# Kernel optimization log

Hardware: AMD Instinct MI355X
Metric: run time of the kernel (lower is better)

Reference implementation:

```python
import jax, jax.numpy as jnp
import numpy as np
import math

N_ENT, N_USR, N_EDGE, C = 100000, 50000, 1000000, 64
N_FACT, N_REL, N_HOPS = 4, 10, 2
KG_HEADS = 2
TEMP = 0.2


def scatter_softmax(scores, seg, num_segments):
    m = jax.ops.segment_max(scores, seg, num_segments=num_segments)
    e = jnp.exp(scores - m[seg])
    s = jax.ops.segment_sum(e, seg, num_segments=num_segments)
    return e / (s[seg] + 1e-16)


def l2norm(x, eps=1e-12):
    n = jnp.linalg.norm(x, axis=-1, keepdims=True)
    return x / jnp.maximum(n, eps)


def setup_inputs() -> dict:
    key = jax.random.key(0)
    ks = jax.random.split(key, 12)
    return {
        "user_emb": jax.random.normal(ks[0], (N_USR, C), jnp.float32) * 0.1,
        "entity_emb": jax.random.normal(ks[1], (N_ENT, C), jnp.float32) * 0.1,
        "latent_emb": jax.random.normal(ks[2], (N_FACT, C), jnp.float32) * 0.1,
        "weight": jax.random.normal(ks[3], (N_REL - 1, C), jnp.float32) * 0.1,
        "disen_weight_att": jax.random.normal(ks[4], (N_FACT, N_REL - 1), jnp.float32) * 0.1,
        "kg_W_r": jax.random.normal(ks[5], (C, C), jnp.float32) * 0.1,
        "ui_vals": jax.random.uniform(ks[6], (N_EDGE,), jnp.float32),
        "edge_index": jax.random.randint(ks[7], (2, N_EDGE), 0, N_ENT, jnp.int64 if jax.config.read('jax_enable_x64') else jnp.int32),
        "edge_type": jax.random.randint(ks[8], (N_EDGE,), 1, N_REL, jnp.int32),
        "ui_rows": jax.random.randint(ks[9], (N_EDGE,), 0, N_USR, jnp.int32),
        "ui_cols": jax.random.randint(ks[10], (N_EDGE,), 0, N_ENT, jnp.int32),
    }


def reference(user_emb, entity_emb, latent_emb, weight, disen_weight_att,
              kg_W_r, ui_vals, edge_index, edge_type, ui_rows, ui_cols):
    head, tail = edge_index[0], edge_index[1]
    d_k = C // KG_HEADS

    # ---- _cul_cor with ind == 'mi' ----
    disen_T = disen_weight_att.T  # [R-1, F]
    nT = disen_T / jnp.linalg.norm(disen_T, axis=1, keepdims=True)
    pos = jnp.sum(nT * nT, axis=1)
    ttl = jnp.sum(disen_T @ disen_weight_att, axis=1)
    cor = -jnp.sum(jnp.log(jnp.exp(pos / TEMP) / jnp.exp(ttl / TEMP)))

    # ---- Invariant_Capture (g_mask=None) ----
    rel_emb = weight[edge_type - 1]          # [E, C]
    head_emb = entity_emb[head]              # [E, C]
    q = (head_emb @ kg_W_r).reshape(-1, KG_HEADS, d_k)
    k = (rel_emb @ kg_W_r).reshape(-1, KG_HEADS, d_k)
    score_r = ((q * k).sum(-1) / math.sqrt(d_k)).mean(-1)  # [E]
    rel_scores = scatter_softmax(score_r, head, N_ENT)
    t_emb = entity_emb[tail]
    r_emb = rel_emb * rel_scores[:, None]
    # bmm of concat(h,r) with concat(t,r) == h.t + r.r
    score_trip = (head_emb * t_emb).sum(-1) + (r_emb * r_emb).sum(-1)
    kg_mask = scatter_softmax(score_trip, head, N_ENT)  # invariant_mask [E]

    # ---- conv_compute: n_hops Aggregator layers, no dropout (eval-determinism) ----
    counts = jnp.clip(jax.ops.segment_sum(jnp.ones_like(kg_mask), head,
                                          num_segments=N_ENT), 1.0)
    disen_w = jax.nn.softmax(disen_weight_att, axis=-1) @ weight  # [F, C]

    ent, usr = entity_emb, user_emb
    ent_res, usr_res = entity_emb, user_emb
    for _ in range(N_HOPS):
        # KG aggregate: scatter_mean over head of masked tail*relation messages
        neigh = ent[tail] * weight[edge_type - 1] * kg_mask[:, None]  # [E, C]
        ent_agg = jax.ops.segment_sum(neigh, head, num_segments=N_ENT) / counts[:, None]
        # user->factor attention on current user embedding
        score = jax.nn.softmax(usr @ latent_emb.T, axis=1)[:, :, None]  # [U, F, 1]
        # sparse user aggregation: interact_mat @ ent
        u_agg = jax.ops.segment_sum(ent[ui_cols] * ui_vals[:, None], ui_rows,
                                    num_segments=N_USR)
        mix = (disen_w[None, :, :] * score).sum(axis=1)  # [U, C]
        u_agg = u_agg * mix + u_agg
        ent = l2norm(ent_agg)
        usr = l2norm(u_agg)
        ent_res = ent_res + ent
        usr_res = usr_res + usr
    return ent_res, usr_res, cor
```

## Files before the change

### kernel.cpp

```cpp
#include <hip/hip_runtime.h>
#include <math.h>

#define N_ENT 100000
#define N_USR 50000
#define N_EDGE 1000000
#define TEMPC 0.2f
#define KG_BLOCKS (N_ENT / 4)
#define UI_BLOCKS (N_USR / 4)

#define TB_BLOCKS 6250
#define CNT_BLOCKS 489
#define SC_BLOCKS 196

#define BIN_BLOCKS 245
#define NCK 391
#define NCU 196
#define FINEK_BLOCKS NCK
#define FINEU_BLOCKS NCU

#define WLS 68

typedef unsigned short ushort_t;

__device__ __forceinline__ float waveReduceSum(float x) {
#pragma unroll
  for (int d = 32; d > 0; d >>= 1) x += __shfl_xor(x, d);
  return x;
}
__device__ __forceinline__ float waveReduceMax(float x) {
#pragma unroll
  for (int d = 32; d > 0; d >>= 1) x = fmaxf(x, __shfl_xor(x, d));
  return x;
}
__device__ __forceinline__ int waveReduceSumI(int x) {
#pragma unroll
  for (int d = 32; d > 0; d >>= 1) x += __shfl_xor(x, d);
  return x;
}
__device__ __forceinline__ float bf2f(unsigned int u16) {
  union { unsigned int i; float f; } v;
  v.i = u16 << 16;
  return v.f;
}
__device__ __forceinline__ ushort_t f2bf(float f) {
  union { unsigned int i; float f; } v;
  v.f = f;
  unsigned int u = v.i;
  u = (u + 0x7FFFu + ((u >> 16) & 1u)) >> 16;
  return (ushort_t)u;
}
__device__ __forceinline__ int rl(int v, int l) { return __builtin_amdgcn_readlane(v, l); }
__device__ __forceinline__ float rlf(float v, int l) {
  return __int_as_float(__builtin_amdgcn_readlane(__float_as_int(v), l));
}

__device__ __forceinline__ float colRT(float a0, float a1, float a2, float a3,
                                       float a4, float a5, float a6, float a7,
                                       int g, int part) {
#define RED3(x) x += __shfl_xor(x, 8); x += __shfl_xor(x, 16); x += __shfl_xor(x, 32);
  RED3(a0) RED3(a1) RED3(a2) RED3(a3) RED3(a4) RED3(a5) RED3(a6) RED3(a7)
#undef RED3
  float t0 = __shfl(a0, g), t1 = __shfl(a1, g), t2 = __shfl(a2, g), t3 = __shfl(a3, g);
  float t4 = __shfl(a4, g), t5 = __shfl(a5, g), t6 = __shfl(a6, g), t7 = __shfl(a7, g);
  float r = t0;
  r = (part == 1) ? t1 : r;
  r = (part == 2) ? t2 : r;
  r = (part == 3) ? t3 : r;
  r = (part == 4) ? t4 : r;
  r = (part == 5) ? t5 : r;
  r = (part == 6) ? t6 : r;
  r = (part == 7) ? t7 : r;
  return r;
}

__global__ void k_pre(const float* __restrict__ ent0, ushort_t* __restrict__ ent0bf,
                      const int* __restrict__ head, const int* __restrict__ uir,
                      int* __restrict__ ccnt_kg, int* __restrict__ ccnt_ui,
                      const float* __restrict__ weight, const float* __restrict__ kgW,
                      const float* __restrict__ disen,
                      float* __restrict__ V, float* __restrict__ wsq,
                      float* __restrict__ dw, float* __restrict__ cor_out,
                      const float* __restrict__ user_emb, const float* __restrict__ latent,
                      float4* __restrict__ sc4a) {
  int bid = blockIdx.x;
  if (bid < TB_BLOCKS) {
    int i = bid * 256 + threadIdx.x;
    if (i < N_ENT * 16) {
      float4 v = ((const float4*)ent0)[i];
      ushort4 o;
      o.x = f2bf(v.x); o.y = f2bf(v.y); o.z = f2bf(v.z); o.w = f2bf(v.w);
      ((ushort4*)ent0bf)[i] = o;
    }
  } else if (bid < TB_BLOCKS + CNT_BLOCKS) {
    __shared__ int histK[NCK], histU[NCU];
    int tid = threadIdx.x;
    for (int i = tid; i < NCK; i += 256) histK[i] = 0;
    for (int i = tid; i < NCU; i += 256) histU[i] = 0;
    __syncthreads();
    int i0 = ((bid - TB_BLOCKS) * 256 + tid) * 8;
    if (i0 < N_EDGE) {
      int4 ha = *(const int4*)(head + i0), hb = *(const int4*)(head + i0 + 4);
      int4 ua = *(const int4*)(uir + i0), ub = *(const int4*)(uir + i0 + 4);
      atomicAdd(&histK[ha.x >> 8], 1);
      atomicAdd(&histK[ha.y >> 8], 1);
      atomicAdd(&histK[ha.z >> 8], 1);
      atomicAdd(&histK[ha.w >> 8], 1);
      atomicAdd(&histK[hb.x >> 8], 1);
      atomicAdd(&histK[hb.y >> 8], 1);
      atomicAdd(&histK[hb.z >> 8], 1);
      atomicAdd(&histK[hb.w >> 8], 1);
      atomicAdd(&histU[ua.x >> 8], 1);
      atomicAdd(&histU[ua.y >> 8], 1);
      atomicAdd(&histU[ua.z >> 8], 1);
      atomicAdd(&histU[ua.w >> 8], 1);
      atomicAdd(&histU[ub.x >> 8], 1);
      atomicAdd(&histU[ub.y >> 8], 1);
      atomicAdd(&histU[ub.z >> 8], 1);
      atomicAdd(&histU[ub.w >> 8], 1);
    }
    __syncthreads();
    for (int i = tid; i < NCK; i += 256)
      if (histK[i] > 0) atomicAdd(&ccnt_kg[i], histK[i]);
    for (int i = tid; i < NCU; i += 256)
      if (histU[i] > 0) atomicAdd(&ccnt_ui[i], histU[i]);
  } else if (bid == TB_BLOCKS + CNT_BLOCKS) {
    __shared__ float T[9 * 64];
    __shared__ float sm[4 * 9];
    int tid = threadIdx.x;
    for (int e = tid; e < 9 * 64; e += 256) {
      int r = e >> 6, d = e & 63;
      float s = 0.f;
      for (int k = 0; k < 64; ++k) s += kgW[k * 64 + d] * weight[r * 64 + k];
      T[e] = s;
    }
    if (tid < 4) {
      float m = -INFINITY;
      for (int r = 0; r < 9; ++r) m = fmaxf(m, disen[tid * 9 + r]);
      float den = 0.f;
      float ex[9];
      for (int r = 0; r < 9; ++r) { ex[r] = expf(disen[tid * 9 + r] - m); den += ex[r]; }
      for (int r = 0; r < 9; ++r) sm[tid * 9 + r] = ex[r] / den;
    }
    __syncthreads();
    for (int e = tid; e < 9 * 64; e += 256) {
      int r = e >> 6, i = e & 63;
      float s = 0.f;
      for (int d = 0; d < 64; ++d) s += kgW[i * 64 + d] * T[r * 64 + d];
      V[e] = s;
    }
    if (tid < 9) {
      float s = 0.f;
      for (int c = 0; c < 64; ++c) { float w = weight[tid * 64 + c]; s += w * w; }
      wsq[tid] = s;
    }
    for (int e = tid; e < 4 * 64; e += 256) {
      int f = e >> 6, c = e & 63;
      float s = 0.f;
      for (int r = 0; r < 9; ++r) s += sm[f * 9 + r] * weight[r * 64 + c];
      dw[e] = s;
    }
    if (tid == 0) {
// ... 179 lines not shown
    __syncthreads();
    int pre9[9];
    int deg = 0;
    if (tid < ne) {
#pragma unroll
      for (int r = 0; r < 9; ++r) { pre9[r] = deg; deg += lcnt[tid * 9 + r]; }
    }
    int x = deg;
#pragma unroll
    for (int d = 1; d < 64; d <<= 1) {
      int y = __shfl_up(x, d);
      if (lane >= d) x += y;
    }
    if (lane == 63) woff[wid] = x;
    __syncthreads();
    if (tid == 0) {
      int a = 0;
      for (int w2 = 0; w2 < 4; ++w2) { int t = woff[w2]; woff[w2] = a; a += t; }
    }
    __syncthreads();
    int ebase = cs + (x - deg) + woff[wid];
    if (tid < ne) {
      head_ptr[gb + tid] = ebase;
#pragma unroll
      for (int r = 0; r < 9; ++r) lbase[tid * 9 + r] = ebase + pre9[r];
    }
    __syncthreads();
    for (int i = tid; i < 2304; i += 256) lcnt[i] = 0;
    __syncthreads();
    for (int i = cs + tid; i < ce; i += 256) {
      unsigned int w = stage_kg[i];
      int key = (int)((w >> 24) & 255u) * 9 + (int)((w >> 20) & 15u);
      int r = atomicAdd(&lcnt[key], 1);
      packed[lbase[key] + r] = (int)(w & 0xFFFFFFu);
    }
    __syncthreads();
    if (tid < ne) {
      int ent = gb + tid;
      float a[9] = {0, 0, 0, 0, 0, 0, 0, 0, 0};
      const uint4* row = (const uint4*)(ent0bf + ((size_t)ent << 6));
#pragma unroll
      for (int q = 0; q < 8; ++q) {
        uint4 bq = row[q];
        float ch0 = bf2f(bq.x & 0xFFFFu), ch1 = bf2f(bq.x >> 16);
        float ch2 = bf2f(bq.y & 0xFFFFu), ch3 = bf2f(bq.y >> 16);
        float ch4 = bf2f(bq.z & 0xFFFFu), ch5 = bf2f(bq.z >> 16);
        float ch6 = bf2f(bq.w & 0xFFFFu), ch7 = bf2f(bq.w >> 16);
#pragma unroll
        for (int r = 0; r < 9; ++r) {
          const float4* vp = (const float4*)(Vl + r * 64 + q * 8);
          float4 v0 = vp[0], v1 = vp[1];
          float t = a[r];
          t = fmaf(ch0, v0.x, t); t = fmaf(ch1, v0.y, t);
          t = fmaf(ch2, v0.z, t); t = fmaf(ch3, v0.w, t);
          t = fmaf(ch4, v1.x, t); t = fmaf(ch5, v1.y, t);
          t = fmaf(ch6, v1.z, t); t = fmaf(ch7, v1.w, t);
          a[r] = t;
        }
      }
      const float inv2s = 0.08838834764831845f;
      int cnt[9];
#pragma unroll
      for (int r = 0; r < 9; ++r) cnt[r] = lcnt[tid * 9 + r];
      float m1 = -INFINITY;
#pragma unroll
      for (int r = 0; r < 9; ++r)
        if (cnt[r] > 0) m1 = fmaxf(m1, a[r] * inv2s);
      if (m1 == -INFINITY) {
#pragma unroll
        for (int r = 0; r < 9; ++r) rel2t[ent * 9 + r] = 0.f;
      } else {
        float den1 = 1e-16f;
#pragma unroll
        for (int r = 0; r < 9; ++r)
          if (cnt[r] > 0) den1 += (float)cnt[r] * expf(a[r] * inv2s - m1);
#pragma unroll
        for (int r = 0; r < 9; ++r) {
          float rs = expf(a[r] * inv2s - m1) / den1;
          rel2t[ent * 9 + r] = rs * rs * wsql[r];
        }
      }
    }
  } else {
    int b = blockIdx.x - FINEK_BLOCKS;
    __shared__ int lbu[256];
    __shared__ int lcu[256];
    __shared__ int woff2[4];
    lcu[tid] = 0;
    int cs = cbase_ui[b], ce = cbase_ui[b + 1];
    int gb = b << 8;
    int nu = min(256, N_USR - gb);
    __syncthreads();
    for (int i = cs + tid; i < ce; i += 256) {
      int2 d = stage_ui[i];
      atomicAdd(&lcu[(d.x >> 24) & 255], 1);
    }
    __syncthreads();
    int deg = (tid < nu) ? lcu[tid] : 0;
    int x = deg;
#pragma unroll
    for (int d = 1; d < 64; d <<= 1) {
      int y = __shfl_up(x, d);
      if (lane >= d) x += y;
    }
    if (lane == 63) woff2[wid] = x;
    __syncthreads();
    if (tid == 0) {
      int a = 0;
      for (int w2 = 0; w2 < 4; ++w2) { int t = woff2[w2]; woff2[w2] = a; a += t; }
    }
    __syncthreads();
    int ubase = cs + (x - deg) + woff2[wid];
    __syncthreads();
    if (tid < nu) {
      ui_ptr[gb + tid] = ubase;
      lbu[tid] = ubase;
    }
    lcu[tid] = 0;
    __syncthreads();
    for (int i = cs + tid; i < ce; i += 256) {
      int2 d = stage_ui[i];
      int key = (d.x >> 24) & 255;
      int r = atomicAdd(&lcu[key], 1);
      cv[lbu[key] + r] = make_int2(d.x & 0xFFFFFF, d.y);
    }
  }
}

__device__ __forceinline__ float kg_agg64(int deg, int lane, int pk, float mk,
                                          const ushort_t* __restrict__ srcbf,
                                          const float* __restrict__ wl) {
  float a0 = 0.f, a1 = 0.f, a2 = 0.f, a3 = 0.f;
  int j = 0;
  for (; j + 4 <= deg; j += 4) {
    int p0 = rl(pk, j), p1 = rl(pk, j + 1), p2 = rl(pk, j + 2), p3 = rl(pk, j + 3);
    float k0 = rlf(mk, j), k1 = rlf(mk, j + 1), k2 = rlf(mk, j + 2), k3 = rlf(mk, j + 3);
    float r0 = bf2f(srcbf[((p0 & 0xFFFFF) << 6) + lane]);
    float r1 = bf2f(srcbf[((p1 & 0xFFFFF) << 6) + lane]);
    float r2 = bf2f(srcbf[((p2 & 0xFFFFF) << 6) + lane]);
    float r3 = bf2f(srcbf[((p3 & 0xFFFFF) << 6) + lane]);
    a0 = fmaf(r0 * wl[((p0 >> 20) & 15) * WLS + lane], k0, a0);
    a1 = fmaf(r1 * wl[((p1 >> 20) & 15) * WLS + lane], k1, a1);
    a2 = fmaf(r2 * wl[((p2 >> 20) & 15) * WLS + lane], k2, a2);
    a3 = fmaf(r3 * wl[((p3 >> 20) & 15) * WLS + lane], k3, a3);
  }
  for (; j < deg; ++j) {
    int pj = rl(pk, j);
    float kj = rlf(mk, j);
    a0 = fmaf(bf2f(srcbf[((pj & 0xFFFFF) << 6) + lane]) * wl[((pj >> 20) & 15) * WLS + lane], kj, a0);
  }
  return (a0 + a1) + (a2 + a3);
}

__device__ __forceinline__ void ui_body(int usr, int lane,
                                        const ushort_t* __restrict__ srcbf,
                                        const float4* __restrict__ sc4,
                                        const float* __restrict__ addb,
                                        float* __restrict__ outp, float* __restrict__ nxt,
                                        const int* __restrict__ uptr,
                                        const int2* __restrict__ cv,
                                        const float* __restrict__ dwl,
                                        const float* __restrict__ latl,
                                        float4* __restrict__ sc4out) {
  float4 s4 = sc4[usr];
  float m = fmaxf(fmaxf(s4.x, s4.y), fmaxf(s4.z, s4.w));
  float e0 = expf(s4.x - m), e1 = expf(s4.y - m), e2 = expf(s4.z - m), e3 = expf(s4.w - m);
  float den = e0 + e1 + e2 + e3;
  float mix = (e0 * dwl[lane] + e1 * dwl[64 + lane] + e2 * dwl[128 + lane] + e3 * dwl[192 + lane]) / den;
  int s = uptr[usr], e = uptr[usr + 1];
  int g = lane >> 3, part = lane & 7;
  float a0 = 0.f, a1 = 0.f, a2 = 0.f, a3 = 0.f;
  float a4 = 0.f, a5 = 0.f, a6 = 0.f, a7 = 0.f;
  for (int base = s; base < e; base += 64) {
    int c = min(64, e - base);
    int2 cvl = (lane < c) ? cv[base + lane] : make_int2(0, 0);
    int cl = cvl.x;
    float vl = __int_as_float(cvl.y);
    int nch = (c + 7) >> 3;
#pragma unroll
    for (int cc = 0; cc < 8; ++cc) {
      if (cc < nch) {
        int j = (cc << 3) + g;
        int cj = __shfl(cl, j);
        float vj = __shfl(vl, j);
        uint4 b = *((const uint4*)(srcbf + ((size_t)cj << 6)) + part);
        a0 = fmaf(bf2f(b.x & 0xFFFFu), vj, a0);
        a1 = fmaf(bf2f(b.x >> 16), vj, a1);
        a2 = fmaf(bf2f(b.y & 0xFFFFu), vj, a2);
        a3 = fmaf(bf2f(b.y >> 16), vj, a3);
        a4 = fmaf(bf2f(b.z & 0xFFFFu), vj, a4);
        a5 = fmaf(bf2f(b.z >> 16), vj, a5);
        a6 = fmaf(bf2f(b.w & 0xFFFFu), vj, a6);
        a7 = fmaf(bf2f(b.w >> 16), vj, a7);
      }
    }
  }
  float acc = colRT(a0, a1, a2, a3, a4, a5, a6, a7, g, part);
  float ua = acc * mix + acc;
  float nrm = sqrtf(waveReduceSum(ua * ua));
  float val = ua / fmaxf(nrm, 1e-12f);
  size_t o = (size_t)usr * 64 + lane;
  if (nxt) nxt[o] = val;
  outp[o] = addb[o] + val;
  if (sc4out) {
    float s0 = waveReduceSum(val * latl[lane]);
    float s1 = waveReduceSum(val * latl[64 + lane]);
    float s2 = waveReduceSum(val * latl[128 + lane]);
    float s3 = waveReduceSum(val * latl[192 + lane]);
    if (lane == 0) sc4out[usr] = make_float4(s0, s1, s2, s3);
  }
}

__global__ void k_mask_kg_ui(const float* __restrict__ ent0,
                             const ushort_t* __restrict__ ent0bf,
                             const int* __restrict__ hptr, const int* __restrict__ packed,
                             const float* __restrict__ rel2t,
                             float* __restrict__ mask_s, const float* __restrict__ weight,
                             float* __restrict__ out_ent, ushort_t* __restrict__ ent1bf,
                             const float4* __restrict__ sc4,
                             float* __restrict__ out_usr,
                             float* __restrict__ usr1, const int* __restrict__ uptr,
                             const int2* __restrict__ cv,
                             const float* __restrict__ user_emb, const float* __restrict__ dw,
                             const float* __restrict__ latent, float4* __restrict__ sc4b) {
  int lane = threadIdx.x & 63, wid = threadIdx.x >> 6;
  if (blockIdx.x < KG_BLOCKS) {
    __shared__ __align__(16) float sh_eh[4][64];
    __shared__ __align__(16) float wl[9 * WLS];
    for (int i = threadIdx.x; i < 576; i += 256) wl[(i >> 6) * WLS + (i & 63)] = weight[i];
    int ent = blockIdx.x * 4 + wid;
    int s = hptr[ent], e = hptr[ent + 1];
    float eh = ent0[(size_t)ent * 64 + lane];
    sh_eh[wid][lane] = eh;
    __syncthreads();
    size_t o = (size_t)ent * 64 + lane;
    int deg = e - s;
    if (deg == 0) {
      ent1bf[o] = f2bf(0.f);
      out_ent[o] = eh;
      return;
    }
    if (deg <= 64) {
      int pk = (lane < deg) ? packed[s + lane] : 0;
      int tb = (pk >> 20) & 15;
      float r2sel = rel2t[ent * 9 + ((lane < deg) ? tb : 0)];
      int g = lane >> 3, part = lane & 7;
      const float4* ehq = (const float4*)(sh_eh[wid] + (part << 3));
      float4 ef0 = ehq[0], ef1 = ehq[1];
      int nch = (deg + 7) >> 3;
      float den = 0.f;
      float acc0 = 0.f, acc1 = 0.f, acc2 = 0.f, acc3 = 0.f;
      float acc4 = 0.f, acc5 = 0.f, acc6 = 0.f, acc7 = 0.f;
      float ws8[8];
#pragma unroll
      for (int cc = 0; cc < 8; ++cc) {
        ws8[cc] = 0.f;
        if (cc < nch) {
          int j = (cc << 3) + g;
          int pkj = __shfl(pk, j);
          uint4 b = *((const uint4*)(ent0bf + ((size_t)(pkj & 0xFFFFF) << 6)) + part);
          float r0 = bf2f(b.x & 0xFFFFu), r1 = bf2f(b.x >> 16);
          float r2 = bf2f(b.y & 0xFFFFu), r3 = bf2f(b.y >> 16);
          float r4 = bf2f(b.z & 0xFFFFu), r5 = bf2f(b.z >> 16);
          float r6 = bf2f(b.w & 0xFFFFu), r7 = bf2f(b.w >> 16);
          float s0 = r0 * ef0.x, s1 = r2 * ef0.z, s2 = r4 * ef1.x, s3 = r6 * ef1.z;
          s0 = fmaf(r1, ef0.y, s0); s1 = fmaf(r3, ef0.w, s1);
          s2 = fmaf(r5, ef1.y, s2); s3 = fmaf(r7, ef1.w, s3);
          float sv = (s0 + s1) + (s2 + s3);
          sv += __shfl_xor(sv, 1);
          sv += __shfl_xor(sv, 2);
          sv += __shfl_xor(sv, 4);
          float r2j = __shfl(r2sel, j);
          float w = (j < deg) ? expf(sv + r2j) : 0.f;
          ws8[cc] = w;
          den += w;
          const float4* wp = (const float4*)(wl + ((pkj >> 20) & 15) * WLS + (part << 3));
          float4 w0 = wp[0], w1 = wp[1];
          acc0 = fmaf(w * r0, w0.x, acc0);
          acc1 = fmaf(w * r1, w0.y, acc1);
          acc2 = fmaf(w * r2, w0.z, acc2);
          acc3 = fmaf(w * r3, w0.w, acc3);
          acc4 = fmaf(w * r4, w1.x, acc4);
          acc5 = fmaf(w * r5, w1.y, acc5);
          acc6 = fmaf(w * r6, w1.z, acc6);
          acc7 = fmaf(w * r7, w1.w, acc7);
        }
      }
      float den2 = den;
      den2 += __shfl_xor(den2, 8);
      den2 += __shfl_xor(den2, 16);
      den2 += __shfl_xor(den2, 32);
      den2 += 1e-16f;
      float invden = 1.0f / den2;
#pragma unroll
      for (int cc = 0; cc < 8; ++cc) {
        if (cc < nch) {
          int j = (cc << 3) + g;
          if (part == 0 && j < deg) mask_s[s + j] = ws8[cc] * invden;
        }
      }
      float aggv = colRT(acc0, acc1, acc2, acc3, acc4, acc5, acc6, acc7, g, part);
      float agg = aggv * invden / (float)deg;
      float nrm = sqrtf(waveReduceSum(agg * agg));
      float val = agg / fmaxf(nrm, 1e-12f);
      ent1bf[o] = f2bf(val);
      out_ent[o] = eh + val;
    } else {
      float m2l = -INFINITY;
      for (int base = s; base < e; base += 64) {
        int c = min(64, e - base);
        int pk = (lane < c) ? packed[base + lane] : 0;
        int tb = (pk >> 20) & 15;
        float r2 = rel2t[ent * 9 + ((lane < c) ? tb : 0)];
        int tl = pk & 0xFFFFF;
        const uint4* row = (const uint4*)(ent0bf + (tl << 6));
        const float* ehp = sh_eh[wid];
        float d = 0.f;
#pragma unroll
        for (int q = 0; q < 8; ++q) {
          uint4 a = row[q];
          d += bf2f(a.x & 0xFFFF) * ehp[q * 8 + 0] + bf2f(a.x >> 16) * ehp[q * 8 + 1];
          d += bf2f(a.y & 0xFFFF) * ehp[q * 8 + 2] + bf2f(a.y >> 16) * ehp[q * 8 + 3];
          d += bf2f(a.z & 0xFFFF) * ehp[q * 8 + 4] + bf2f(a.z >> 16) * ehp[q * 8 + 5];
          d += bf2f(a.w & 0xFFFF) * ehp[q * 8 + 6] + bf2f(a.w >> 16) * ehp[q * 8 + 7];
        }
        float trip = d + r2;
        if (lane < c) {
          mask_s[base + lane] = trip;
          m2l = fmaxf(m2l, trip);
        }
      }
      float m2 = waveReduceMax(m2l);
      float denl = 0.f;
      for (int base = s; base < e; base += 64) {
        int c = min(64, e - base);
        denl += (lane < c) ? expf(mask_s[base + lane] - m2) : 0.f;
      }
      float den2 = waveReduceSum(denl) + 1e-16f;
      float acc = 0.f;
      for (int base = s; base < e; base += 64) {
        int c = min(64, e - base);
        int pk = (lane < c) ? packed[base + lane] : 0;
        float mk = 0.f;
        if (lane < c) {
          mk = expf(mask_s[base + lane] - m2) / den2;
          mask_s[base + lane] = mk;
        }
        acc += kg_agg64(c, lane, pk, mk, ent0bf, wl);
      }
      float agg = acc / (float)deg;
      float nrm = sqrtf(waveReduceSum(agg * agg));
      float val = agg / fmaxf(nrm, 1e-12f);
      ent1bf[o] = f2bf(val);
      out_ent[o] = eh + val;
    }
  } else {
    __shared__ float dwl[256];
    __shared__ float latl[256];
    if (threadIdx.x < 256) {
      dwl[threadIdx.x] = dw[threadIdx.x];
      latl[threadIdx.x] = latent[threadIdx.x];
    }
    __syncthreads();
    int usr = (blockIdx.x - KG_BLOCKS) * 4 + wid;
    ui_body(usr, lane, ent0bf, sc4, user_emb, out_usr, usr1,
            uptr, cv, dwl, latl, sc4b);
  }
}

__global__ void k_hop2(const ushort_t* __restrict__ srcbf,
                       float* __restrict__ out_ent,
                       const int* __restrict__ hptr, const int* __restrict__ packed,
                       const float* __restrict__ mask_s, const float* __restrict__ weight,
                       const float* __restrict__ usr1, float* __restrict__ out_usr,
                       const int* __restrict__ uptr, const int2* __restrict__ cv,
                       const float4* __restrict__ sc4,
                       const float* __restrict__ dw) {
  int lane = threadIdx.x & 63, wid = threadIdx.x >> 6;
  if (blockIdx.x < KG_BLOCKS) {
    __shared__ __align__(16) float wl[9 * WLS];
    for (int i = threadIdx.x; i < 576; i += 256) wl[(i >> 6) * WLS + (i & 63)] = weight[i];
    __syncthreads();
    int ent = blockIdx.x * 4 + wid;
    int s = hptr[ent], e = hptr[ent + 1];
    int g = lane >> 3, part = lane & 7;
    float a0 = 0.f, a1 = 0.f, a2 = 0.f, a3 = 0.f;
    float a4 = 0.f, a5 = 0.f, a6 = 0.f, a7 = 0.f;
    for (int base = s; base < e; base += 64) {
      int c = min(64, e - base);
      int pk = (lane < c) ? packed[base + lane] : 0;
      float mk = (lane < c) ? mask_s[base + lane] : 0.f;
      int nch = (c + 7) >> 3;
#pragma unroll
      for (int cc = 0; cc < 8; ++cc) {
        if (cc < nch) {
          int j = (cc << 3) + g;
          int pkj = __shfl(pk, j);
          float mkj = __shfl(mk, j);
          uint4 b = *((const uint4*)(srcbf + ((size_t)(pkj & 0xFFFFF) << 6)) + part);
          float r0 = bf2f(b.x & 0xFFFFu), r1 = bf2f(b.x >> 16);
          float r2 = bf2f(b.y & 0xFFFFu), r3 = bf2f(b.y >> 16);
          float r4 = bf2f(b.z & 0xFFFFu), r5 = bf2f(b.z >> 16);
          float r6 = bf2f(b.w & 0xFFFFu), r7 = bf2f(b.w >> 16);
          const float4* wp = (const float4*)(wl + ((pkj >> 20) & 15) * WLS + (part << 3));
          float4 w0 = wp[0], w1 = wp[1];
          a0 = fmaf(mkj * r0, w0.x, a0);
          a1 = fmaf(mkj * r1, w0.y, a1);
          a2 = fmaf(mkj * r2, w0.z, a2);
          a3 = fmaf(mkj * r3, w0.w, a3);
          a4 = fmaf(mkj * r4, w1.x, a4);
          a5 = fmaf(mkj * r5, w1.y, a5);
          a6 = fmaf(mkj * r6, w1.z, a6);
          a7 = fmaf(mkj * r7, w1.w, a7);
        }
      }
    }
    float aggv = colRT(a0, a1, a2, a3, a4, a5, a6, a7, g, part);
    float n = (float)(e - s);
    float agg = aggv / fmaxf(n, 1.0f);
    float nrm = sqrtf(waveReduceSum(agg * agg));
    float val = agg / fmaxf(nrm, 1e-12f);
    size_t o = (size_t)ent * 64 + lane;
    out_ent[o] = out_ent[o] + val;
  } else {
    __shared__ float dwl[256];
    if (threadIdx.x < 256) dwl[threadIdx.x] = dw[threadIdx.x];
    __syncthreads();
    int usr = (blockIdx.x - KG_BLOCKS) * 4 + wid;
    ui_body(usr, lane, srcbf, sc4, out_usr, out_usr, nullptr,
            uptr, cv, dwl, nullptr, nullptr);
  }
}

extern "C" void kernel_launch(void* const* d_in, const int* in_sizes, int n_in,
                              void* d_out, int out_size, void* d_ws, size_t ws_size,
                              hipStream_t stream) {
  const float* user_emb = (const float*)d_in[0];
  const float* entity_emb = (const float*)d_in[1];
  const float* latent = (const float*)d_in[2];
  const float* weight = (const float*)d_in[3];
  const float* disen = (const float*)d_in[4];
  const float* kgW = (const float*)d_in[5];
  const float* ui_vals = (const float*)d_in[6];
  const int* edge_index = (const int*)d_in[7];
  const int* edge_type = (const int*)d_in[8];
  const int* ui_rows = (const int*)d_in[9];
  const int* ui_cols = (const int*)d_in[10];
  const int* head = edge_index;
  const int* tail = edge_index + N_EDGE;

  char* ws = (char*)d_ws;
  size_t o = 0;
  auto alloc = [&](size_t bytes) -> char* {
    char* p = ws + o;
    o += (bytes + 255) & ~(size_t)255;
    return p;
  };
  int* head_ptr = (int*)alloc((N_ENT + 1) * 4);
  int* ui_ptr = (int*)alloc((N_USR + 1) * 4);
  int* packed = (int*)alloc((size_t)N_EDGE * 4);
  int2* cv = (int2*)alloc((size_t)N_EDGE * 8);
  float* mask_s = (float*)alloc((size_t)N_EDGE * 4);
  ushort_t* ent0bf = (ushort_t*)alloc((size_t)N_ENT * 64 * 2);
  ushort_t* ent1bf = (ushort_t*)alloc((size_t)N_ENT * 64 * 2);
  float* usr1 = (float*)alloc((size_t)N_USR * 64 * 4);
  unsigned int* stage_kg = (unsigned int*)alloc((size_t)N_EDGE * 4);
  int2* stage_ui = (int2*)alloc((size_t)N_EDGE * 8);
  int* ccnt = (int*)alloc((NCK + NCU) * 4);
  int* ccnt_kg = ccnt;
  int* ccnt_ui = ccnt + NCK;
  int* cbase_kg = (int*)alloc((NCK + 1) * 4);
  int* cbase_ui = (int*)alloc((NCU + 1) * 4);
  int* cur_kg = (int*)alloc(NCK * 4);
  int* cur_ui = (int*)alloc(NCU * 4);
  float* rel2t = (float*)alloc((size_t)N_ENT * 9 * 4);
  float4* sc4a = (float4*)alloc((size_t)N_USR * 16);
  float4* sc4b = (float4*)alloc((size_t)N_USR * 16);
  float* V = (float*)alloc(9 * 64 * 4);
  float* wsq = (float*)alloc(16 * 4);
  float* dw = (float*)alloc(4 * 64 * 4);
  if (o > ws_size) return;

  float* out_ent = (float*)d_out;
  float* out_usr = out_ent + (size_t)N_ENT * 64;
  float* out_cor = out_ent + (size_t)N_ENT * 64 + (size_t)N_USR * 64;

  hipMemsetAsync(ccnt, 0, (NCK + NCU) * 4, stream);

  k_pre<<<TB_BLOCKS + CNT_BLOCKS + 1 + SC_BLOCKS, 256, 0, stream>>>(
      entity_emb, ent0bf, head, ui_rows, ccnt_kg, ccnt_ui,
      weight, kgW, disen, V, wsq, dw, out_cor, user_emb, latent, sc4a);

  k_scan_coarse<<<1, 1024, 0, stream>>>(ccnt_kg, ccnt_ui, cbase_kg, cbase_ui,
                                        cur_kg, cur_ui, head_ptr, ui_ptr);

  k_bin<<<BIN_BLOCKS, 1024, 0, stream>>>(
      head, tail, edge_type, ui_rows, ui_cols, ui_vals,
      cur_kg, cur_ui, stage_kg, stage_ui);

  k_fine_rel2<<<FINEK_BLOCKS + FINEU_BLOCKS, 256, 0, stream>>>(
      stage_kg, stage_ui, cbase_kg, cbase_ui, packed, cv,
      head_ptr, ui_ptr, ent0bf, V, wsq, rel2t);

  k_mask_kg_ui<<<KG_BLOCKS + UI_BLOCKS, 256, 0, stream>>>(
      entity_emb, ent0bf, head_ptr, packed, rel2t, mask_s, weight,
      out_ent, ent1bf, sc4a, out_usr, usr1, ui_ptr, cv, user_emb, dw, latent, sc4b);

  k_hop2<<<KG_BLOCKS + UI_BLOCKS, 256, 0, stream>>>(
      ent1bf, out_ent, head_ptr, packed, mask_s, weight,
      usr1, out_usr, ui_ptr, cv, sc4b, dw);
}
```

Before: 405.4 us.

## Process four rows per wavefront with software-prefetched edge lists in hop kernels

```diff
diff --git a/kernel.cpp b/kernel.cpp
--- a/kernel.cpp
+++ b/kernel.cpp
@@ -5,8 +5,8 @@
 #define N_USR 50000
 #define N_EDGE 1000000
 #define TEMPC 0.2f
-#define KG_BLOCKS (N_ENT / 4)
-#define UI_BLOCKS (N_USR / 4)
+#define KG_BLOCKS 6250
+#define UI_BLOCKS 3125
 
 #define TB_BLOCKS 6250
 #define CNT_BLOCKS 489
@@ -492,30 +492,154 @@
   return (a0 + a1) + (a2 + a3);
 }
 
-__device__ __forceinline__ void ui_body(int usr, int lane,
-                                        const ushort_t* __restrict__ srcbf,
-                                        const float4* __restrict__ sc4,
-                                        const float* __restrict__ addb,
-                                        float* __restrict__ outp, float* __restrict__ nxt,
-                                        const int* __restrict__ uptr,
-                                        const int2* __restrict__ cv,
-                                        const float* __restrict__ dwl,
-                                        const float* __restrict__ latl,
-                                        float4* __restrict__ sc4out) {
+__device__ __forceinline__ void kg_one(
+    int ent, int s, int deg, int pk_pre, float eh, int lane, int wid,
+    float (*sh_eh)[64], const float* __restrict__ wl,
+    const ushort_t* __restrict__ ent0bf, const int* __restrict__ packed,
+    const float* __restrict__ rel2t, float* __restrict__ mask_s,
+    float* __restrict__ out_ent, ushort_t* __restrict__ ent1bf) {
+  size_t o = (size_t)ent * 64 + lane;
+  if (deg == 0) {
+    ent1bf[o] = f2bf(0.f);
+    out_ent[o] = eh;
+    return;
+  }
+  sh_eh[wid][lane] = eh;
+  int e = s + deg;
+  if (deg <= 64) {
+    int pk = pk_pre;
+    int tb = (pk >> 20) & 15;
+    float r2sel = rel2t[ent * 9 + ((lane < deg) ? tb : 0)];
+    int g = lane >> 3, part = lane & 7;
+    const float4* ehq = (const float4*)(sh_eh[wid] + (part << 3));
+    float4 ef0 = ehq[0], ef1 = ehq[1];
+    int nch = (deg + 7) >> 3;
+    float den = 0.f;
+    float acc0 = 0.f, acc1 = 0.f, acc2 = 0.f, acc3 = 0.f;
+    float acc4 = 0.f, acc5 = 0.f, acc6 = 0.f, acc7 = 0.f;
+    float ws8[8];
+#pragma unroll
+    for (int cc = 0; cc < 8; ++cc) {
+      ws8[cc] = 0.f;
+      if (cc < nch) {
+        int j = (cc << 3) + g;
+        int pkj = __shfl(pk, j);
+        uint4 b = *((const uint4*)(ent0bf + ((size_t)(pkj & 0xFFFFF) << 6)) + part);
+        float r0 = bf2f(b.x & 0xFFFFu), r1 = bf2f(b.x >> 16);
+        float r2 = bf2f(b.y & 0xFFFFu), r3 = bf2f(b.y >> 16);
+        float r4 = bf2f(b.z & 0xFFFFu), r5 = bf2f(b.z >> 16);
+        float r6 = bf2f(b.w & 0xFFFFu), r7 = bf2f(b.w >> 16);
+        float s0 = r0 * ef0.x, s1 = r2 * ef0.z, s2 = r4 * ef1.x, s3 = r6 * ef1.z;
+        s0 = fmaf(r1, ef0.y, s0); s1 = fmaf(r3, ef0.w, s1);
+        s2 = fmaf(r5, ef1.y, s2); s3 = fmaf(r7, ef1.w, s3);
+        float sv = (s0 + s1) + (s2 + s3);
+        sv += __shfl_xor(sv, 1);
+        sv += __shfl_xor(sv, 2);
+        sv += __shfl_xor(sv, 4);
+        float r2j = __shfl(r2sel, j);
+        float w = (j < deg) ? expf(sv + r2j) : 0.f;
+        ws8[cc] = w;
+        den += w;
+        const float4* wp = (const float4*)(wl + ((pkj >> 20) & 15) * WLS + (part << 3));
+        float4 w0 = wp[0], w1 = wp[1];
+        acc0 = fmaf(w * r0, w0.x, acc0);
+        acc1 = fmaf(w * r1, w0.y, acc1);
+        acc2 = fmaf(w * r2, w0.z, acc2);
+        acc3 = fmaf(w * r3, w0.w, acc3);
+        acc4 = fmaf(w * r4, w1.x, acc4);
+        acc5 = fmaf(w * r5, w1.y, acc5);
+        acc6 = fmaf(w * r6, w1.z, acc6);
+        acc7 = fmaf(w * r7, w1.w, acc7);
+      }
+    }
+    float den2 = den;
+    den2 += __shfl_xor(den2, 8);
+    den2 += __shfl_xor(den2, 16);
+    den2 += __shfl_xor(den2, 32);
+    den2 += 1e-16f;
+    float invden = 1.0f / den2;
+#pragma unroll
+    for (int cc = 0; cc < 8; ++cc) {
+      if (cc < nch) {
+        int j = (cc << 3) + (lane >> 3);
+        if ((lane & 7) == 0 && j < deg) mask_s[s + j] = ws8[cc] * invden;
+      }
+    }
+    float aggv = colRT(acc0, acc1, acc2, acc3, acc4, acc5, acc6, acc7, g, part);
+    float agg = aggv * invden / (float)deg;
+    float nrm = sqrtf(waveReduceSum(agg * agg));
+    float val = agg / fmaxf(nrm, 1e-12f);
+    ent1bf[o] = f2bf(val);
+    out_ent[o] = eh + val;
+  } else {
+    float m2l = -INFINITY;
+    for (int base = s; base < e; base += 64) {
+      int c = min(64, e - base);
+      int pk = (lane < c) ? packed[base + lane] : 0;
+      int tb = (pk >> 20) & 15;
+      float r2 = rel2t[ent * 9 + ((lane < c) ? tb : 0)];
+      int tl = pk & 0xFFFFF;
+      const uint4* row = (const uint4*)(ent0bf + (tl << 6));
+      const float* ehp = sh_eh[wid];
+      float d = 0.f;
+#pragma unroll
+      for (int q = 0; q < 8; ++q) {
+        uint4 a = row[q];
+        d += bf2f(a.x & 0xFFFF) * ehp[q * 8 + 0] + bf2f(a.x >> 16) * ehp[q * 8 + 1];
+        d += bf2f(a.y & 0xFFFF) * ehp[q * 8 + 2] + bf2f(a.y >> 16) * ehp[q * 8 + 3];
+        d += bf2f(a.z & 0xFFFF) * ehp[q * 8 + 4] + bf2f(a.z >> 16) * ehp[q * 8 + 5];
+        d += bf2f(a.w & 0xFFFF) * ehp[q * 8 + 6] + bf2f(a.w >> 16) * ehp[q * 8 + 7];
+      }
+      float trip = d + r2;
+      if (lane < c) {
+        mask_s[base + lane] = trip;
+        m2l = fmaxf(m2l, trip);
+      }
+    }
+    float m2 = waveReduceMax(m2l);
+    float denl = 0.f;
+    for (int base = s; base < e; base += 64) {
+      int c = min(64, e - base);
+      denl += (lane < c) ? expf(mask_s[base + lane] - m2) : 0.f;
+    }
+    float den2 = waveReduceSum(denl) + 1e-16f;
+    float acc = 0.f;
+    for (int base = s; base < e; base += 64) {
+      int c = min(64, e - base);
+      int pk = (lane < c) ? packed[base + lane] : 0;
+      float mk = 0.f;
+      if (lane < c) {
+        mk = expf(mask_s[base + lane] - m2) / den2;
+        mask_s[base + lane] = mk;
+      }
+      acc += kg_agg64(c, lane, pk, mk, ent0bf, wl);
+    }
+    float agg = acc / (float)deg;
+    float nrm = sqrtf(waveReduceSum(agg * agg));
+    float val = agg / fmaxf(nrm, 1e-12f);
+    ent1bf[o] = f2bf(val);
+    out_ent[o] = eh + val;
+  }
+}
+
+__device__ __forceinline__ void ui_one(
+    int usr, int lane, int s, int e, int2 cvl0,
+    const ushort_t* __restrict__ srcbf, const float4* __restrict__ sc4,
+    const float* __restrict__ addb, float* __restrict__ outp, float* __restrict__ nxt,
+    const int2* __restrict__ cv, const float* __restrict__ dwl,
+    const float* __restrict__ latl, float4* __restrict__ sc4out) {
   float4 s4 = sc4[usr];
   float m = fmaxf(fmaxf(s4.x, s4.y), fmaxf(s4.z, s4.w));
   float e0 = expf(s4.x - m), e1 = expf(s4.y - m), e2 = expf(s4.z - m), e3 = expf(s4.w - m);
   float den = e0 + e1 + e2 + e3;
   float mix = (e0 * dwl[lane] + e1 * dwl[64 + lane] + e2 * dwl[128 + lane] + e3 * dwl[192 + lane]) / den;
-  int s = uptr[usr], e = uptr[usr + 1];
   int g = lane >> 3, part = lane & 7;
   float a0 = 0.f, a1 = 0.f, a2 = 0.f, a3 = 0.f;
   float a4 = 0.f, a5 = 0.f, a6 = 0.f, a7 = 0.f;
-  for (int base = s; base < e; base += 64) {
-    int c = min(64, e - base);
-    int2 cvl = (lane < c) ? cv[base + lane] : make_int2(0, 0);
-    int cl = cvl.x;
-    float vl = __int_as_float(cvl.y);
+  {
+    int c = min(64, e - s);
+    int cl = cvl0.x;
+    float vl = __int_as_float(cvl0.y);
     int nch = (c + 7) >> 3;
 #pragma unroll
     for (int cc = 0; cc < 8; ++cc) {
@@ -535,6 +659,30 @@
       }
     }
   }
+  for (int base = s + 64; base < e; base += 64) {
+    int c = min(64, e - base);
+    int2 cvl = (lane < c) ? cv[base + lane] : make_int2(0, 0);
+    int cl = cvl.x;
+    float vl = __int_as_float(cvl.y);
+    int nch = (c + 7) >> 3;
+#pragma unroll
+    for (int cc = 0; cc < 8; ++cc) {
+      if (cc < nch) {
+        int j = (cc << 3) + g;
+        int cj = __shfl(cl, j);
+        float vj = __shfl(vl, j);
+        uint4 b = *((const uint4*)(srcbf + ((size_t)cj << 6)) + part);
+        a0 = fmaf(bf2f(b.x & 0xFFFFu), vj, a0);
+        a1 = fmaf(bf2f(b.x >> 16), vj, a1);
+        a2 = fmaf(bf2f(b.y & 0xFFFFu), vj, a2);
+        a3 = fmaf(bf2f(b.y >> 16), vj, a3);
+        a4 = fmaf(bf2f(b.z & 0xFFFFu), vj, a4);
+        a5 = fmaf(bf2f(b.z >> 16), vj, a5);
+        a6 = fmaf(bf2f(b.w & 0xFFFFu), vj, a6);
+        a7 = fmaf(bf2f(b.w >> 16), vj, a7);
+      }
+    }
+  }
   float acc = colRT(a0, a1, a2, a3, a4, a5, a6, a7, g, part);
   float ua = acc * mix + acc;
   float nrm = sqrtf(waveReduceSum(ua * ua));
@@ -549,6 +697,78 @@
     float s3 = waveReduceSum(val * latl[192 + lane]);
     if (lane == 0) sc4out[usr] = make_float4(s0, s1, s2, s3);
   }
+}
+
+__device__ __forceinline__ void kg2_one(
+    int ent, int lane, int s, int e, int pk0, float mk0, float prev,
+    const ushort_t* __restrict__ srcbf, const int* __restrict__ packed,
+    const float* __restrict__ mask_s, const float* __restrict__ wl,
+    float* __restrict__ out_ent) {
+  int g = lane >> 3, part = lane & 7;
+  float a0 = 0.f, a1 = 0.f, a2 = 0.f, a3 = 0.f;
+  float a4 = 0.f, a5 = 0.f, a6 = 0.f, a7 = 0.f;
+  {
+    int c = min(64, e - s);
+    int nch = (c + 7) >> 3;
+#pragma unroll
+    for (int cc = 0; cc < 8; ++cc) {
+      if (cc < nch) {
+        int j = (cc << 3) + g;
+        int pkj = __shfl(pk0, j);
+        float mkj = __shfl(mk0, j);
+        uint4 b = *((const uint4*)(srcbf + ((size_t)(pkj & 0xFFFFF) << 6)) + part);
+        float r0 = bf2f(b.x & 0xFFFFu), r1 = bf2f(b.x >> 16);
+        float r2 = bf2f(b.y & 0xFFFFu), r3 = bf2f(b.y >> 16);
+        float r4 = bf2f(b.z & 0xFFFFu), r5 = bf2f(b.z >> 16);
+        float r6 = bf2f(b.w & 0xFFFFu), r7 = bf2f(b.w >> 16);
+        const float4* wp = (const float4*)(wl + ((pkj >> 20) & 15) * WLS + (part << 3));
+        float4 w0 = wp[0], w1 = wp[1];
+        a0 = fmaf(mkj * r0, w0.x, a0);
+        a1 = fmaf(mkj * r1, w0.y, a1);
+        a2 = fmaf(mkj * r2, w0.z, a2);
+        a3 = fmaf(mkj * r3, w0.w, a3);
+        a4 = fmaf(mkj * r4, w1.x, a4);
+        a5 = fmaf(mkj * r5, w1.y, a5);
+        a6 = fmaf(mkj * r6, w1.z, a6);
+        a7 = fmaf(mkj * r7, w1.w, a7);
+      }
+    }
+  }
+  for (int base = s + 64; base < e; base += 64) {
+    int c = min(64, e - base);
+    int pk = (lane < c) ? packed[base + lane] : 0;
+    float mk = (lane < c) ? mask_s[base + lane] : 0.f;
+    int nch = (c + 7) >> 3;
+#pragma unroll
+    for (int cc = 0; cc < 8; ++cc) {
+      if (cc < nch) {
+        int j = (cc << 3) + g;
+        int pkj = __shfl(pk, j);
+        float mkj = __shfl(mk, j);
+        uint4 b = *((const uint4*)(srcbf + ((size_t)(pkj & 0xFFFFF) << 6)) + part);
+        float r0 = bf2f(b.x & 0xFFFFu), r1 = bf2f(b.x >> 16);
+        float r2 = bf2f(b.y & 0xFFFFu), r3 = bf2f(b.y >> 16);
+        float r4 = bf2f(b.z & 0xFFFFu), r5 = bf2f(b.z >> 16);
+        float r6 = bf2f(b.w & 0xFFFFu), r7 = bf2f(b.w >> 16);
+        const float4* wp = (const float4*)(wl + ((pkj >> 20) & 15) * WLS + (part << 3));
+        float4 w0 = wp[0], w1 = wp[1];
+        a0 = fmaf(mkj * r0, w0.x, a0);
+        a1 = fmaf(mkj * r1, w0.y, a1);
+        a2 = fmaf(mkj * r2, w0.z, a2);
+        a3 = fmaf(mkj * r3, w0.w, a3);
+        a4 = fmaf(mkj * r4, w1.x, a4);
+        a5 = fmaf(mkj * r5, w1.y, a5);
+        a6 = fmaf(mkj * r6, w1.z, a6);
+        a7 = fmaf(mkj * r7, w1.w, a7);
+      }
+    }
+  }
+  float aggv = colRT(a0, a1, a2, a3, a4, a5, a6, a7, g, part);
+  float n = (float)(e - s);
+  float agg = aggv / fmaxf(n, 1.0f);
+  float nrm = sqrtf(waveReduceSum(agg * agg));
+  float val = agg / fmaxf(nrm, 1e-12f);
+  out_ent[(size_t)ent * 64 + lane] = prev + val;
 }
 
 __global__ void k_mask_kg_ui(const float* __restrict__ ent0,
@@ -568,132 +788,27 @@
     __shared__ __align__(16) float sh_eh[4][64];
     __shared__ __align__(16) float wl[9 * WLS];
     for (int i = threadIdx.x; i < 576; i += 256) wl[(i >> 6) * WLS + (i & 63)] = weight[i];
-    int ent = blockIdx.x * 4 + wid;
-    int s = hptr[ent], e = hptr[ent + 1];
-    float eh = ent0[(size_t)ent * 64 + lane];
-    sh_eh[wid][lane] = eh;
-    __syncthreads();
-    size_t o = (size_t)ent * 64 + lane;
-    int deg = e - s;
-    if (deg == 0) {
-      ent1bf[o] = f2bf(0.f);
-      out_ent[o] = eh;
-      return;
-    }
-    if (deg <= 64) {
-      int pk = (lane < deg) ? packed[s + lane] : 0;
-      int tb = (pk >> 20) & 15;
-      float r2sel = rel2t[ent * 9 + ((lane < deg) ? tb : 0)];
-      int g = lane >> 3, part = lane & 7;
-      const float4* ehq = (const float4*)(sh_eh[wid] + (part << 3));
-      float4 ef0 = ehq[0], ef1 = ehq[1];
-      int nch = (deg + 7) >> 3;
-      float den = 0.f;
-      float acc0 = 0.f, acc1 = 0.f, acc2 = 0.f, acc3 = 0.f;
-      float acc4 = 0.f, acc5 = 0.f, acc6 = 0.f, acc7 = 0.f;
-      float ws8[8];
-#pragma unroll
-      for (int cc = 0; cc < 8; ++cc) {
-        ws8[cc] = 0.f;
-        if (cc < nch) {
-          int j = (cc << 3) + g;
-          int pkj = __shfl(pk, j);
-          uint4 b = *((const uint4*)(ent0bf + ((size_t)(pkj & 0xFFFFF) << 6)) + part);
-          float r0 = bf2f(b.x & 0xFFFFu), r1 = bf2f(b.x >> 16);
-          float r2 = bf2f(b.y & 0xFFFFu), r3 = bf2f(b.y >> 16);
-          float r4 = bf2f(b.z & 0xFFFFu), r5 = bf2f(b.z >> 16);
-          float r6 = bf2f(b.w & 0xFFFFu), r7 = bf2f(b.w >> 16);
-          float s0 = r0 * ef0.x, s1 = r2 * ef0.z, s2 = r4 * ef1.x, s3 = r6 * ef1.z;
-          s0 = fmaf(r1, ef0.y, s0); s1 = fmaf(r3, ef0.w, s1);
-          s2 = fmaf(r5, ef1.y, s2); s3 = fmaf(r7, ef1.w, s3);
-          float sv = (s0 + s1) + (s2 + s3);
-          sv += __shfl_xor(sv, 1);
-          sv += __shfl_xor(sv, 2);
-          sv += __shfl_xor(sv, 4);
-          float r2j = __shfl(r2sel, j);
-          float w = (j < deg) ? expf(sv + r2j) : 0.f;
-          ws8[cc] = w;
-          den += w;
-          const float4* wp = (const float4*)(wl + ((pkj >> 20) & 15) * WLS + (part << 3));
-          float4 w0 = wp[0], w1 = wp[1];
-          acc0 = fmaf(w * r0, w0.x, acc0);
-          acc1 = fmaf(w * r1, w0.y, acc1);
-          acc2 = fmaf(w * r2, w0.z, acc2);
-          acc3 = fmaf(w * r3, w0.w, acc3);
-          acc4 = fmaf(w * r4, w1.x, acc4);
-          acc5 = fmaf(w * r5, w1.y, acc5);
-          acc6 = fmaf(w * r6, w1.z, acc6);
-          acc7 = fmaf(w * r7, w1.w, acc7);
-        }
-      }
-      float den2 = den;
-      den2 += __shfl_xor(den2, 8);
-      den2 += __shfl_xor(den2, 16);
-      den2 += __shfl_xor(den2, 32);
-      den2 += 1e-16f;
-      float invden = 1.0f / den2;
-#pragma unroll
-      for (int cc = 0; cc < 8; ++cc) {
-        if (cc < nch) {
-          int j = (cc << 3) + g;
-          if (part == 0 && j < deg) mask_s[s + j] = ws8[cc] * invden;
-        }
-      }
-      float aggv = colRT(acc0, acc1, acc2, acc3, acc4, acc5, acc6, acc7, g, part);
-      float agg = aggv * invden / (float)deg;
-      float nrm = sqrtf(waveReduceSum(agg * agg));
-      float val = agg / fmaxf(nrm, 1e-12f);
-      ent1bf[o] = f2bf(val);
-      out_ent[o] = eh + val;
-    } else {
-      float m2l = -INFINITY;
-      for (int base = s; base < e; base += 64) {
-        int c = min(64, e - base);
-        int pk = (lane < c) ? packed[base + lane] : 0;
-        int tb = (pk >> 20) & 15;
-        float r2 = rel2t[ent * 9 + ((lane < c) ? tb : 0)];
-        int tl = pk & 0xFFFFF;
-        const uint4* row = (const uint4*)(ent0bf + (tl << 6));
-        const float* ehp = sh_eh[wid];
-        float d = 0.f;
-#pragma unroll
-        for (int q = 0; q < 8; ++q) {
-          uint4 a = row[q];
-          d += bf2f(a.x & 0xFFFF) * ehp[q * 8 + 0] + bf2f(a.x >> 16) * ehp[q * 8 + 1];
-          d += bf2f(a.y & 0xFFFF) * ehp[q * 8 + 2] + bf2f(a.y >> 16) * ehp[q * 8 + 3];
-          d += bf2f(a.z & 0xFFFF) * ehp[q * 8 + 4] + bf2f(a.z >> 16) * ehp[q * 8 + 5];
-          d += bf2f(a.w & 0xFFFF) * ehp[q * 8 + 6] + bf2f(a.w >> 16) * ehp[q * 8 + 7];
-        }
-        float trip = d + r2;
-        if (lane < c) {
-          mask_s[base + lane] = trip;
-          m2l = fmaxf(m2l, trip);
-        }
-      }
-      float m2 = waveReduceMax(m2l);
-      float denl = 0.f;
-      for (int base = s; base < e; base += 64) {
-        int c = min(64, e - base);
-        denl += (lane < c) ? expf(mask_s[base + lane] - m2) : 0.f;
-      }
-      float den2 = waveReduceSum(denl) + 1e-16f;
-      float acc = 0.f;
-      for (int base = s; base < e; base += 64) {
-        int c = min(64, e - base);
-        int pk = (lane < c) ? packed[base + lane] : 0;
-        float mk = 0.f;
-        if (lane < c) {
-          mk = expf(mask_s[base + lane] - m2) / den2;
-          mask_s[base + lane] = mk;
-        }
-        acc += kg_agg64(c, lane, pk, mk, ent0bf, wl);
-      }
-      float agg = acc / (float)deg;
-      float nrm = sqrtf(waveReduceSum(agg * agg));
-      float val = agg / fmaxf(nrm, 1e-12f);
-      ent1bf[o] = f2bf(val);
-      out_ent[o] = eh + val;
-    }
+    __syncthreads();
+    int e0 = (blockIdx.x * 4 + wid) * 4;
+    int hp = (lane < 5) ? hptr[e0 + lane] : 0;
+    int s0 = rl(hp, 0), s1 = rl(hp, 1), s2 = rl(hp, 2), s3 = rl(hp, 3), s4 = rl(hp, 4);
+    int dA = s1 - s0, dB = s2 - s1, dC = s3 - s2, dD = s4 - s3;
+    float ehA = ent0[(size_t)e0 * 64 + lane];
+    int pkA = (dA <= 64 && lane < dA) ? packed[s0 + lane] : 0;
+    float ehB = ent0[(size_t)(e0 + 1) * 64 + lane];
+    int pkB = (dB <= 64 && lane < dB) ? packed[s1 + lane] : 0;
+    kg_one(e0 + 0, s0, dA, pkA, ehA, lane, wid, sh_eh, wl, ent0bf, packed,
+           rel2t, mask_s, out_ent, ent1bf);
+    float ehC = ent0[(size_t)(e0 + 2) * 64 + lane];
+    int pkC = (dC <= 64 && lane < dC) ? packed[s2 + lane] : 0;
+    kg_one(e0 + 1, s1, dB, pkB, ehB, lane, wid, sh_eh, wl, ent0bf, packed,
+           rel2t, mask_s, out_ent, ent1bf);
+    float ehD = ent0[(size_t)(e0 + 3) * 64 + lane];
+    int pkD = (dD <= 64 && lane < dD) ? packed[s3 + lane] : 0;
+    kg_one(e0 + 2, s2, dC, pkC, ehC, lane, wid, sh_eh, wl, ent0bf, packed,
+           rel2t, mask_s, out_ent, ent1bf);
+    kg_one(e0 + 3, s3, dD, pkD, ehD, lane, wid, sh_eh, wl, ent0bf, packed,
+           rel2t, mask_s, out_ent, ent1bf);
   } else {
     __shared__ float dwl[256];
     __shared__ float latl[256];
@@ -702,9 +817,25 @@
       latl[threadIdx.x] = latent[threadIdx.x];
     }
     __syncthreads();
-    int usr = (blockIdx.x - KG_BLOCKS) * 4 + wid;
-    ui_body(usr, lane, ent0bf, sc4, user_emb, out_usr, usr1,
-            uptr, cv, dwl, latl, sc4b);
+    int u0 = ((blockIdx.x - KG_BLOCKS) * 4 + wid) * 4;
+    int up = (lane < 5) ? uptr[u0 + lane] : 0;
+    int t0 = rl(up, 0), t1 = rl(up, 1), t2 = rl(up, 2), t3 = rl(up, 3), t4 = rl(up, 4);
+    int cA = min(64, t1 - t0);
+    int2 cvA = (lane < cA) ? cv[t0 + lane] : make_int2(0, 0);
+    int cB = min(64, t2 - t1);
+    int2 cvB = (lane < cB) ? cv[t1 + lane] : make_int2(0, 0);
+    ui_one(u0 + 0, lane, t0, t1, cvA, ent0bf, sc4, user_emb, out_usr, usr1,
+           cv, dwl, latl, sc4b);
+    int cC = min(64, t3 - t2);
+    int2 cvC = (lane < cC) ? cv[t2 + lane] : make_int2(0, 0);
+    ui_one(u0 + 1, lane, t1, t2, cvB, ent0bf, sc4, user_emb, out_usr, usr1,
+           cv, dwl, latl, sc4b);
+    int cD = min(64, t4 - t3);
+    int2 cvD = (lane < cD) ? cv[t3 + lane] : make_int2(0, 0);
+    ui_one(u0 + 2, lane, t2, t3, cvC, ent0bf, sc4, user_emb, out_usr, usr1,
+           cv, dwl, latl, sc4b);
+    ui_one(u0 + 3, lane, t3, t4, cvD, ent0bf, sc4, user_emb, out_usr, usr1,
+           cv, dwl, latl, sc4b);
   }
 }
 
@@ -721,54 +852,52 @@
     __shared__ __align__(16) float wl[9 * WLS];
     for (int i = threadIdx.x; i < 576; i += 256) wl[(i >> 6) * WLS + (i & 63)] = weight[i];
     __syncthreads();
-    int ent = blockIdx.x * 4 + wid;
-    int s = hptr[ent], e = hptr[ent + 1];
-    int g = lane >> 3, part = lane & 7;
-    float a0 = 0.f, a1 = 0.f, a2 = 0.f, a3 = 0.f;
-    float a4 = 0.f, a5 = 0.f, a6 = 0.f, a7 = 0.f;
-    for (int base = s; base < e; base += 64) {
-      int c = min(64, e - base);
-      int pk = (lane < c) ? packed[base + lane] : 0;
-      float mk = (lane < c) ? mask_s[base + lane] : 0.f;
-      int nch = (c + 7) >> 3;
-#pragma unroll
-      for (int cc = 0; cc < 8; ++cc) {
-        if (cc < nch) {
-          int j = (cc << 3) + g;
-          int pkj = __shfl(pk, j);
-          float mkj = __shfl(mk, j);
-          uint4 b = *((const uint4*)(srcbf + ((size_t)(pkj & 0xFFFFF) << 6)) + part);
-          float r0 = bf2f(b.x & 0xFFFFu), r1 = bf2f(b.x >> 16);
-          float r2 = bf2f(b.y & 0xFFFFu), r3 = bf2f(b.y >> 16);
-          float r4 = bf2f(b.z & 0xFFFFu), r5 = bf2f(b.z >> 16);
-          float r6 = bf2f(b.w & 0xFFFFu), r7 = bf2f(b.w >> 16);
-          const float4* wp = (const float4*)(wl + ((pkj >> 20) & 15) * WLS + (part << 3));
-          float4 w0 = wp[0], w1 = wp[1];
-          a0 = fmaf(mkj * r0, w0.x, a0);
-          a1 = fmaf(mkj * r1, w0.y, a1);
-          a2 = fmaf(mkj * r2, w0.z, a2);
-          a3 = fmaf(mkj * r3, w0.w, a3);
-          a4 = fmaf(mkj * r4, w1.x, a4);
-          a5 = fmaf(mkj * r5, w1.y, a5);
-          a6 = fmaf(mkj * r6, w1.z, a6);
-          a7 = fmaf(mkj * r7, w1.w, a7);
-        }
-      }
-    }
-    float aggv = colRT(a0, a1, a2, a3, a4, a5, a6, a7, g, part);
-    float n = (float)(e - s);
-    float agg = aggv / fmaxf(n, 1.0f);
-    float nrm = sqrtf(waveReduceSum(agg * agg));
-    float val = agg / fmaxf(nrm, 1e-12f);
-    size_t o = (size_t)ent * 64 + lane;
-    out_ent[o] = out_ent[o] + val;
+    int e0 = (blockIdx.x * 4 + wid) * 4;
+    int hp = (lane < 5) ? hptr[e0 + lane] : 0;
+    int s0 = rl(hp, 0), s1 = rl(hp, 1), s2 = rl(hp, 2), s3 = rl(hp, 3), s4 = rl(hp, 4);
+    int cA = min(64, s1 - s0);
+    int pkA = (lane < cA) ? packed[s0 + lane] : 0;
+    float mkA = (lane < cA) ? mask_s[s0 + lane] : 0.f;
+    float pvA = out_ent[(size_t)e0 * 64 + lane];
+    int cB = min(64, s2 - s1);
+    int pkB = (lane < cB) ? packed[s1 + lane] : 0;
+    float mkB = (lane < cB) ? mask_s[s1 + lane] : 0.f;
+    float pvB = out_ent[(size_t)(e0 + 1) * 64 + lane];
+    kg2_one(e0 + 0, lane, s0, s1, pkA, mkA, pvA, srcbf, packed, mask_s, wl, out_ent);
+    int cC = min(64, s3 - s2);
+    int pkC = (lane < cC) ? packed[s2 + lane] : 0;
+    float mkC = (lane < cC) ? mask_s[s2 + lane] : 0.f;
+    float pvC = out_ent[(size_t)(e0 + 2) * 64 + lane];
+    kg2_one(e0 + 1, lane, s1, s2, pkB, mkB, pvB, srcbf, packed, mask_s, wl, out_ent);
+    int cD = min(64, s4 - s3);
+    int pkD = (lane < cD) ? packed[s3 + lane] : 0;
+    float mkD = (lane < cD) ? mask_s[s3 + lane] : 0.f;
+    float pvD = out_ent[(size_t)(e0 + 3) * 64 + lane];
+    kg2_one(e0 + 2, lane, s2, s3, pkC, mkC, pvC, srcbf, packed, mask_s, wl, out_ent);
+    kg2_one(e0 + 3, lane, s3, s4, pkD, mkD, pvD, srcbf, packed, mask_s, wl, out_ent);
   } else {
     __shared__ float dwl[256];
     if (threadIdx.x < 256) dwl[threadIdx.x] = dw[threadIdx.x];
     __syncthreads();
-    int usr = (blockIdx.x - KG_BLOCKS) * 4 + wid;
-    ui_body(usr, lane, srcbf, sc4, out_usr, out_usr, nullptr,
-            uptr, cv, dwl, nullptr, nullptr);
+    int u0 = ((blockIdx.x - KG_BLOCKS) * 4 + wid) * 4;
+    int up = (lane < 5) ? uptr[u0 + lane] : 0;
+    int t0 = rl(up, 0), t1 = rl(up, 1), t2 = rl(up, 2), t3 = rl(up, 3), t4 = rl(up, 4);
+    int cA = min(64, t1 - t0);
+    int2 cvA = (lane < cA) ? cv[t0 + lane] : make_int2(0, 0);
+    int cB = min(64, t2 - t1);
+    int2 cvB = (lane < cB) ? cv[t1 + lane] : make_int2(0, 0);
+    ui_one(u0 + 0, lane, t0, t1, cvA, srcbf, sc4, out_usr, out_usr, nullptr,
+           cv, dwl, nullptr, nullptr);
+    int cC = min(64, t3 - t2);
+    int2 cvC = (lane < cC) ? cv[t2 + lane] : make_int2(0, 0);
+    ui_one(u0 + 1, lane, t1, t2, cvB, srcbf, sc4, out_usr, out_usr, nullptr,
+           cv, dwl, nullptr, nullptr);
+    int cD = min(64, t4 - t3);
+    int2 cvD = (lane < cD) ? cv[t3 + lane] : make_int2(0, 0);
+    ui_one(u0 + 2, lane, t2, t3, cvC, srcbf, sc4, out_usr, out_usr, nullptr,
+           cv, dwl, nullptr, nullptr);
+    ui_one(u0 + 3, lane, t3, t4, cvD, srcbf, sc4, out_usr, out_usr, nullptr,
+           cv, dwl, nullptr, nullptr);
   }
 }
 
```

Result: faster. 394.8 us, median of 2 (-2.6%).
